# Performance work log

Measured on AMD Instinct MI355X. Metric: run time of the kernel, lower is better.

The kernel has to match this reference:

```python
import jax, jax.numpy as jnp
import numpy as np

# Model config (matches init_kwargs)
DIM = 2048
INTER = 1408          # moe_inter_dim
E = 16                # n_routed_experts
TOPK = 4              # n_activated_experts
G = 4                 # n_expert_groups
TOPK_G = 2            # n_limited_groups
N_SHARED = 2
SHARED_INTER = N_SHARED * INTER  # 2816
ROUTE_SCALE = 1.0


def setup_inputs() -> dict:
    key = jax.random.key(0)
    ks = jax.random.split(key, 8)
    s = 0.02
    x = jax.random.normal(ks[0], (1, 2048, DIM), dtype=jnp.float32)
    Wg = jax.random.normal(ks[1], (E, DIM), dtype=jnp.float32) * s      # gate weight
    W1 = jax.random.normal(ks[2], (E, INTER, DIM), dtype=jnp.float32) * s  # expert gate proj
    W3 = jax.random.normal(ks[3], (E, INTER, DIM), dtype=jnp.float32) * s  # expert up proj
    W2 = jax.random.normal(ks[4], (E, DIM, INTER), dtype=jnp.float32) * s  # expert down proj
    Ws1 = jax.random.normal(ks[5], (SHARED_INTER, DIM), dtype=jnp.float32) * s
    Ws3 = jax.random.normal(ks[6], (SHARED_INTER, DIM), dtype=jnp.float32) * s
    Ws2 = jax.random.normal(ks[7], (DIM, SHARED_INTER), dtype=jnp.float32) * s
    return {"x": x, "Wg": Wg, "W1": W1, "W3": W3, "W2": W2,
            "Ws1": Ws1, "Ws3": Ws3, "Ws2": Ws2}


def _moe_forward(x, Wg, W1, W3, W2, Ws1, Ws3, Ws2):
    B, S, D = x.shape
    xt = x.reshape(-1, D)              # [T, D]
    T = xt.shape[0]

    # ---- Gate: group-limited top-k routing (bias is None since dim != 7168) ----
    scores = jax.nn.softmax(xt @ Wg.T, axis=-1)          # [T, E]
    sg = scores.reshape(T, G, E // G)                    # [T, G, E/G]
    group_scores = sg.max(axis=-1)                       # amax per group
    gidx = jax.lax.top_k(group_scores, TOPK_G)[1]        # [T, TOPK_G]
    gmask = jax.nn.one_hot(gidx, G, dtype=jnp.float32).sum(axis=1) > 0  # [T, G] kept groups
    masked = jnp.where(gmask[:, :, None], sg, -jnp.inf).reshape(T, E)
    topi = jax.lax.top_k(masked, TOPK)[1]                # [T, TOPK] expert indices
    weights = jnp.take_along_axis(scores, topi, axis=1) * ROUTE_SCALE  # original_scores gather

    # ---- Routed experts: dense per-expert SwiGLU FFN, zero-weight combine ----
    # combine[t, e] = sum over k of weights[t, k] * (topi[t, k] == e)
    combine = jnp.zeros((T, E), xt.dtype).at[jnp.arange(T)[:, None], topi].add(weights)
    h = jax.nn.silu(jnp.einsum('td,eid->eti', xt, W1)) * jnp.einsum('td,eid->eti', xt, W3)
    expert_out = jnp.einsum('eti,edi->etd', h, W2)       # [E, T, D]
    y = jnp.einsum('etd,te->td', expert_out, combine)    # [T, D]

    # ---- Shared expert (applied to all tokens) ----
    z = (jax.nn.silu(xt @ Ws1.T) * (xt @ Ws3.T)) @ Ws2.T

    return (y + z).reshape(B, S, D)


def reference(x, Wg, W1, W3, W2, Ws1, Ws3, Ws2):
    return _moe_forward(x, Wg, W1, W3, W2, Ws1, Ws3, Ws2)
```

## Files before the change

### kernel.cpp

```cpp
#include <hip/hip_runtime.h>
#include <stdint.h>

#define D_MODEL  2048
#define N_INTER  1408
#define SH_INTER 2816
#define T_TOK    2048
#define NSLOT    (T_TOK * 4)
#define MIB(x)   ((size_t)(x) << 20)

typedef __attribute__((ext_vector_type(8))) short bf16x8;
typedef __attribute__((ext_vector_type(4))) float f32x4;

__device__ __forceinline__ unsigned short f2bf(float f){
  unsigned int b = __builtin_bit_cast(unsigned int, f);
  b = (b + 0x7FFFu + ((b >> 16) & 1u)) >> 16;
  return (unsigned short)b;
}
__device__ __forceinline__ float bf2f(unsigned short h){
  unsigned int b = ((unsigned int)h) << 16;
  return __builtin_bit_cast(float, b);
}

#define GLOAD16(gp, lp) __builtin_amdgcn_global_load_lds( \
    (const __attribute__((address_space(1))) unsigned int*)(gp), \
    (__attribute__((address_space(3))) unsigned int*)(lp), 16, 0, 0)

__global__ void cvt_bf16_kernel(const float* __restrict__ x,
                                unsigned short* __restrict__ o, int n4){
  const int stride = gridDim.x * blockDim.x;
  for (int i = blockIdx.x * blockDim.x + threadIdx.x; i < n4; i += stride){
    const float4 v = ((const float4*)x)[i];
    ushort4 u; u.x = f2bf(v.x); u.y = f2bf(v.y); u.z = f2bf(v.z); u.w = f2bf(v.w);
    ((ushort4*)o)[i] = u;
  }
}

__global__ void gate_kernel(const float* __restrict__ x, const float* __restrict__ Wg,
                            int* __restrict__ cnt, int* __restrict__ list,
                            float* __restrict__ wslot){
  const int t = blockIdx.x;
  const int l = threadIdx.x;
  const int e = l & 15, q = l >> 4;
  const float* xr = x + (size_t)t * D_MODEL + q * 512;
  const float* wr = Wg + (size_t)e * D_MODEL + q * 512;
  float p = 0.f;
  #pragma unroll 4
  for (int i = 0; i < 512; i += 4){
    float4 xv = *(const float4*)(xr + i);
    float4 wv = *(const float4*)(wr + i);
    p += xv.x*wv.x + xv.y*wv.y + xv.z*wv.z + xv.w*wv.w;
  }
  p += __shfl_xor(p, 16);
  p += __shfl_xor(p, 32);
  float mx = p;
  for (int d = 1; d < 16; d <<= 1) mx = fmaxf(mx, __shfl_xor(mx, d));
  float ex = __expf(p - mx);
  float sum = ex;
  for (int d = 1; d < 16; d <<= 1) sum += __shfl_xor(sum, d);
  const float sc = ex / sum;
  float gm = fmaxf(sc, __shfl_xor(sc, 1));
  gm = fmaxf(gm, __shfl_xor(gm, 2));
  const float g0 = __shfl(gm, 0), g1 = __shfl(gm, 4),
              g2 = __shfl(gm, 8), g3 = __shfl(gm, 12);
  const int grp = e >> 2;
  const float gs[4] = {g0, g1, g2, g3};
  int grank = 0;
  #pragma unroll
  for (int j = 0; j < 4; ++j)
    if (gs[j] > gm || (gs[j] == gm && j < grp)) grank++;
  const float msc = (grank < 2) ? sc : -INFINITY;
  int erank = 0;
  #pragma unroll
  for (int j = 0; j < 16; ++j){
    const float oj = __shfl(msc, j);
    if (oj > msc || (oj == msc && j < e)) erank++;
  }
  if (q == 0 && erank < 4 && msc > -INFINITY){
    const int pos = atomicAdd(&cnt[e], 1);
    const int slot = (t << 2) | erank;
    list[e * T_TOK + pos] = slot;
    wslot[slot] = sc;
  }
}

template<int MODE>
__global__ __launch_bounds__(256, 3)
void gemm6_kernel(const unsigned short* __restrict__ A,
                  const unsigned short* __restrict__ B,
                  void* __restrict__ OutP,
                  const int* __restrict__ list,
                  const int* __restrict__ cnt,
                  int N, int K, int Astride, int MT, int NT)
{
  constexpr bool GATHER = (MODE >= 2);
  __shared__ unsigned short As[3 * 128 * 32];
  __shared__ unsigned short Bs[3 * 128 * 32];

  const int per = gridDim.x >> 3;
  const int gsw = (blockIdx.x & 7) * per + (blockIdx.x >> 3);
  const int mt   = gsw % MT;
  const int rest = gsw / MT;
  const int nt = GATHER ? (rest % NT) : rest;
  const int e  = GATHER ? (rest / NT) : 0;

  const int cntE = GATHER ? cnt[e] : (MT * 128);
  if (mt * 128 >= cntE) return;

  const int tid = threadIdx.x, wid = tid >> 6, lane = tid & 63;

  const int rt0 = 32 * wid + (lane >> 2), rt1 = rt0 + 16;
  const int sxA = ((lane & 3) ^ ((lane >> 3) & 3)) << 3;

  int ar0, ar1;
  if constexpr (GATHER){
    const int lim = cntE - 1;
    int p0 = mt * 128 + rt0; p0 = p0 < lim ? p0 : lim;
    int p1 = mt * 128 + rt1; p1 = p1 < lim ? p1 : lim;
    const int e0 = list[e * T_TOK + p0], e1 = list[e * T_TOK + p1];
    ar0 = (MODE == 2) ? (e0 >> 2) : e0;
    ar1 = (MODE == 2) ? (e1 >> 2) : e1;
  } else { ar0 = mt * 128 + rt0; ar1 = mt * 128 + rt1; }

  const unsigned short* pa0 = A + (size_t)ar0 * Astride + sxA;
  const unsigned short* pa1 = A + (size_t)ar1 * Astride + sxA;
  const unsigned short* pb0 = B + (GATHER ? (size_t)e * N * K : 0)
                            + (size_t)(nt * 128 + rt0) * K + sxA;
  const unsigned short* pb1 = pb0 + (size_t)16 * K;

  const int aW0 = (32 * wid) * 32, aW1 = aW0 + 16 * 32;
  const int bufStride = 128 * 32;

  const int wr = wid >> 1, wc = wid & 1, lr = lane & 15, lq = lane >> 4;
  const int fx = ((lq ^ ((lr >> 1) & 3)) << 3);
  int aoff[4], boff[4];
  #pragma unroll
  for (int m = 0; m < 4; ++m) aoff[m] = (wr * 64 + m * 16 + lr) * 32 + fx;
  #pragma unroll
  for (int n = 0; n < 4; ++n) boff[n] = (wc * 64 + n * 16 + lr) * 32 + fx;

  f32x4 acc[4][4];
  const f32x4 zero = {0.f, 0.f, 0.f, 0.f};
  #pragma unroll
  for (int m = 0; m < 4; ++m)
    #pragma unroll
    for (int n = 0; n < 4; ++n) acc[m][n] = zero;

  const int KT = K >> 5;
  #pragma unroll
  for (int t = 0; t < 3; ++t){
    GLOAD16(pa0, As + t * bufStride + aW0);
    GLOAD16(pa1, As + t * bufStride + aW1);
    GLOAD16(pb0, Bs + t * bufStride + aW0);
    GLOAD16(pb1, Bs + t * bufStride + aW1);
    pa0 += 32; pa1 += 32; pb0 += 32; pb1 += 32;
  }
  int c = 0;

  for (int kt = 0; kt < KT; ++kt){
    if (kt < KT - 2)       asm volatile("s_waitcnt vmcnt(8)" ::: "memory");
    else if (kt == KT - 2) asm volatile("s_waitcnt vmcnt(4)" ::: "memory");
    else                   asm volatile("s_waitcnt vmcnt(0)" ::: "memory");
    __builtin_amdgcn_s_barrier();

    const unsigned short* aC = As + c * bufStride;
    const unsigned short* bC = Bs + c * bufStride;
    bf16x8 af[4], bf[4];
    #pragma unroll
    for (int m = 0; m < 4; ++m) af[m] = *(const bf16x8*)(aC + aoff[m]);
    #pragma unroll
    for (int n = 0; n < 4; ++n) bf[n] = *(const bf16x8*)(bC + boff[n]);

    asm volatile("s_waitcnt lgkmcnt(0)" ::: "memory");
    __builtin_amdgcn_sched_barrier(0);
    __builtin_amdgcn_s_barrier();

    if (kt + 3 < KT){
      GLOAD16(pa0, As + c * bufStride + aW0);
      GLOAD16(pa1, As + c * bufStride + aW1);
      GLOAD16(pb0, Bs + c * bufStride + aW0);
      GLOAD16(pb1, Bs + c * bufStride + aW1);
      pa0 += 32; pa1 += 32; pb0 += 32; pb1 += 32;
    }

    #pragma unroll
    for (int n = 0; n < 4; ++n)
      #pragma unroll
      for (int m = 0; m < 4; ++m)
        acc[m][n] = __builtin_amdgcn_mfma_f32_16x16x32_bf16(af[m], bf[n], acc[m][n], 0, 0, 0);

    c = (c == 2) ? 0 : c + 1;
  }

  const int colBase = nt * 128 + wc * 64;
  #pragma unroll
  for (int m = 0; m < 4; ++m){
    #pragma unroll
    for (int r = 0; r < 4; ++r){
      const int grow = mt * 128 + wr * 64 + m * 16 + lq * 4 + r;
      if constexpr (MODE == 1){
        float* op = (float*)OutP + (size_t)grow * N + colBase;
        #pragma unroll
        for (int n = 0; n < 4; ++n) op[n * 16 + lr] = acc[m][n][r];
      } else if constexpr (MODE == 0){
        unsigned short* op = (unsigned short*)OutP + (size_t)grow * N + colBase;
        #pragma unroll
        for (int n = 0; n < 4; ++n) op[n * 16 + lr] = f2bf(acc[m][n][r]);
      } else {
        if (grow >= cntE) continue;
        const int orow = list[e * T_TOK + grow];
        unsigned short* op = (unsigned short*)OutP + (size_t)orow * N + colBase;
        #pragma unroll
        for (int n = 0; n < 4; ++n) op[n * 16 + lr] = f2bf(acc[m][n][r]);
      }
    }
  }
}

__global__ void swiglu_ip_kernel(unsigned short* __restrict__ GU, int n8, int NI8){
  const int stride = gridDim.x * blockDim.x;
  bf16x8* p = (bf16x8*)GU;
  for (int i = blockIdx.x * blockDim.x + threadIdx.x; i < n8; i += stride){
    const int r = i / NI8, ccol = i - r * NI8;
    const size_t gi = (size_t)r * 2 * NI8 + ccol;
    const bf16x8 g = p[gi];
    const bf16x8 u = p[gi + NI8];
    bf16x8 h;
    #pragma unroll
    for (int j = 0; j < 8; ++j){
      const float gv = bf2f((unsigned short)g[j]);
      const float uv = bf2f((unsigned short)u[j]);
      h[j] = (short)f2bf(gv / (1.f + __expf(-gv)) * uv);
    }
    p[gi] = h;
  }
}

__global__ void swiglu2_kernel(unsigned short* __restrict__ G,
                               const unsigned short* __restrict__ U, int n8){
  const int stride = gridDim.x * blockDim.x;
  for (int i = blockIdx.x * blockDim.x + threadIdx.x; i < n8; i += stride){
    const bf16x8 g = ((const bf16x8*)G)[i];
    const bf16x8 u = ((const bf16x8*)U)[i];
    bf16x8 h;
    #pragma unroll
    for (int j = 0; j < 8; ++j){
      const float gv = bf2f((unsigned short)g[j]);
      const float uv = bf2f((unsigned short)u[j]);
      h[j] = (short)f2bf(gv / (1.f + __expf(-gv)) * uv);
    }
    ((bf16x8*)G)[i] = h;
  }
}

__global__ void combine_kernel(const unsigned short* __restrict__ H2,
                               const float* __restrict__ wslot,
                               float* __restrict__ out){
  const int t = blockIdx.x;
  const int ccol = threadIdx.x * 8;
  float w[4];
  #pragma unroll
  for (int k = 0; k < 4; ++k) w[k] = wslot[t * 4 + k];
  float* o = out + (size_t)t * D_MODEL + ccol;
  float a[8];
  #pragma unroll
  for (int j = 0; j < 8; ++j) a[j] = o[j];
  #pragma unroll
  for (int k = 0; k < 4; ++k){
    const bf16x8 hv = *(const bf16x8*)(H2 + (size_t)(t * 4 + k) * D_MODEL + ccol);
    #pragma unroll
    for (int j = 0; j < 8; ++j) a[j] += w[k] * bf2f((unsigned short)hv[j]);
  }
  #pragma unroll
  for (int j = 0; j < 8; ++j) o[j] = a[j];
}

extern "C" void kernel_launch(void* const* d_in, const int* in_sizes, int n_in,
                              void* d_out, int out_size, void* d_ws, size_t ws_size,
                              hipStream_t stream)
{
  const float* x   = (const float*)d_in[0];
  const float* Wg  = (const float*)d_in[1];
  const float* W1  = (const float*)d_in[2];
  const float* W3  = (const float*)d_in[3];
  const float* W2  = (const float*)d_in[4];
  const float* Ws1 = (const float*)d_in[5];
  const float* Ws3 = (const float*)d_in[6];
  const float* Ws2 = (const float*)d_in[7];
  float* out = (float*)d_out;

  char* ws = (char*)d_ws;
  int*   cnt   = (int*)(ws);
  int*   list  = (int*)(ws + 4096);
  float* wslot = (float*)(ws + 4096 + 131072);
  unsigned short* xbf  = (unsigned short*)(ws + MIB(1));
  unsigned short* H2   = (unsigned short*)(ws + MIB(1));
  unsigned short* GU_s = (unsigned short*)(ws + MIB(9));
  unsigned short* Ubuf = (unsigned short*)(ws + MIB(9));
  unsigned short* Wb   = (unsigned short*)(ws + MIB(33));
  unsigned short* Gbuf = (unsigned short*)(ws + MIB(121));
  unsigned short* Wb2  = Wb + (size_t)SH_INTER * D_MODEL;

  hipMemsetAsync(cnt, 0, 4096, stream);
  cvt_bf16_kernel<<<2048, 256, 0, stream>>>(x, xbf, T_TOK * D_MODEL / 4);
  gate_kernel<<<T_TOK, 64, 0, stream>>>(x, Wg, cnt, list, wslot);

  cvt_bf16_kernel<<<4096, 256, 0, stream>>>(Ws1, Wb,  SH_INTER * D_MODEL / 4);
  cvt_bf16_kernel<<<4096, 256, 0, stream>>>(Ws3, Wb2, SH_INTER * D_MODEL / 4);
  gemm6_kernel<0><<<16 * 44, 256, 0, stream>>>(xbf, Wb, GU_s, nullptr, nullptr,
                                               2 * SH_INTER, D_MODEL, D_MODEL, 16, 44);
  swiglu_ip_kernel<<<2048, 256, 0, stream>>>(GU_s, T_TOK * SH_INTER / 8, SH_INTER / 8);
  cvt_bf16_kernel<<<4096, 256, 0, stream>>>(Ws2, Wb, D_MODEL * SH_INTER / 4);
  gemm6_kernel<1><<<16 * 16, 256, 0, stream>>>(GU_s, Wb, out, nullptr, nullptr,
                                               D_MODEL, SH_INTER, 2 * SH_INTER, 16, 16);

  cvt_bf16_kernel<<<8192, 256, 0, stream>>>(W1, Wb, 16 * N_INTER * D_MODEL / 4);
  gemm6_kernel<2><<<16 * 11 * 16, 256, 0, stream>>>(xbf, Wb, Gbuf, list, cnt,
                                                    N_INTER, D_MODEL, D_MODEL, 16, 11);
  cvt_bf16_kernel<<<8192, 256, 0, stream>>>(W3, Wb, 16 * N_INTER * D_MODEL / 4);
  gemm6_kernel<2><<<16 * 11 * 16, 256, 0, stream>>>(xbf, Wb, Ubuf, list, cnt,
                                                    N_INTER, D_MODEL, D_MODEL, 16, 11);
  swiglu2_kernel<<<2048, 256, 0, stream>>>(Gbuf, Ubuf, NSLOT * N_INTER / 8);
  cvt_bf16_kernel<<<8192, 256, 0, stream>>>(W2, Wb, 16 * D_MODEL * N_INTER / 4);
  gemm6_kernel<3><<<16 * 16 * 16, 256, 0, stream>>>(Gbuf, Wb, H2, list, cnt,
                                                    D_MODEL, N_INTER, N_INTER, 16, 16);
  combine_kernel<<<T_TOK, 256, 0, stream>>>(H2, wslot, out);
}
```

Baseline: 604.5 us.

## Move to 256x256 GEMM tiles with fused gate/up, split-K shared down, merged conversions

Replaces the 128x128 GEMM with a 512-thread 256x256-tile variant that raises MFMA priority during the compute phase. The routed W1 and W3 projections are fused into one gathered GEMM whose output holds both halves. The shared down-projection uses 4-way split-K into fp32 partials, which the combine kernel now sums. The x and shared-weight conversions are merged into one launch, and each weight gets its own bf16 buffer instead of reusing one scratch area. These changes aim to cut launch count, improve operand reuse and fill the GPU better, at the cost of more workspace, extra partial-sum traffic, and register pressure from 32 accumulators per thread.

```diff
diff --git a/kernel.cpp b/kernel.cpp
--- a/kernel.cpp
+++ b/kernel.cpp
@@ -32,6 +32,26 @@
     const float4 v = ((const float4*)x)[i];
     ushort4 u; u.x = f2bf(v.x); u.y = f2bf(v.y); u.z = f2bf(v.z); u.w = f2bf(v.w);
     ((ushort4*)o)[i] = u;
+  }
+}
+
+__global__ void cvt4_kernel(const float* __restrict__ x,  const float* __restrict__ Ws1,
+                            const float* __restrict__ Ws3, const float* __restrict__ Ws2,
+                            unsigned short* __restrict__ xbf, unsigned short* __restrict__ S1,
+                            unsigned short* __restrict__ S3,  unsigned short* __restrict__ S2){
+  const int N0 = T_TOK * D_MODEL / 4;
+  const int NW = SH_INTER * D_MODEL / 4;
+  const int total = N0 + 3 * NW;
+  const int stride = gridDim.x * blockDim.x;
+  for (int i = blockIdx.x * blockDim.x + threadIdx.x; i < total; i += stride){
+    const float4* s; ushort4* d; int j;
+    if (i < N0)            { s = (const float4*)x;   d = (ushort4*)xbf; j = i; }
+    else if (i < N0 + NW)  { s = (const float4*)Ws1; d = (ushort4*)S1;  j = i - N0; }
+    else if (i < N0 + 2*NW){ s = (const float4*)Ws3; d = (ushort4*)S3;  j = i - N0 - NW; }
+    else                   { s = (const float4*)Ws2; d = (ushort4*)S2;  j = i - N0 - 2*NW; }
+    const float4 v = s[j];
+    ushort4 u; u.x = f2bf(v.x); u.y = f2bf(v.y); u.z = f2bf(v.z); u.w = f2bf(v.w);
+    d[j] = u;
   }
 }
 
@@ -83,75 +103,87 @@
   }
 }
 
-template<int MODE>
-__global__ __launch_bounds__(256, 3)
-void gemm6_kernel(const unsigned short* __restrict__ A,
-                  const unsigned short* __restrict__ B,
+template<int MODE, int KS>
+__global__ __launch_bounds__(512, 2)
+void gemm8_kernel(const unsigned short* __restrict__ A,
+                  const unsigned short* __restrict__ BG,
+                  const unsigned short* __restrict__ BU,
                   void* __restrict__ OutP,
                   const int* __restrict__ list,
                   const int* __restrict__ cnt,
-                  int N, int K, int Astride, int MT, int NT)
+                  int K, int N, int NI, int MT, int NT)
 {
-  constexpr bool GATHER = (MODE >= 2);
-  __shared__ unsigned short As[3 * 128 * 32];
-  __shared__ unsigned short Bs[3 * 128 * 32];
+  constexpr bool GATHER = (MODE == 2 || MODE == 3);
+  constexpr bool GU     = (MODE == 0 || MODE == 2);
+  __shared__ unsigned short As[3 * 8192];
+  __shared__ unsigned short Bs[3 * 8192];
 
   const int per = gridDim.x >> 3;
   const int gsw = (blockIdx.x & 7) * per + (blockIdx.x >> 3);
-  const int mt   = gsw % MT;
+  const int mt = gsw % MT;
   const int rest = gsw / MT;
-  const int nt = GATHER ? (rest % NT) : rest;
-  const int e  = GATHER ? (rest / NT) : 0;
-
-  const int cntE = GATHER ? cnt[e] : (MT * 128);
-  if (mt * 128 >= cntE) return;
+  const int nt = rest % NT;
+  const int rest2 = rest / NT;
+  const int ks = (KS > 1) ? (rest2 % KS) : 0;
+  const int e  = GATHER ? rest2 : 0;
+  const int cntE = GATHER ? cnt[e] : (MT * 256);
+  if (mt * 256 >= cntE) return;
 
   const int tid = threadIdx.x, wid = tid >> 6, lane = tid & 63;
+  const int sx   = ((lane & 3) ^ ((lane >> 3) & 3)) << 3;
+  const int kOff = (KS > 1) ? ks * (K / KS) : 0;
 
   const int rt0 = 32 * wid + (lane >> 2), rt1 = rt0 + 16;
-  const int sxA = ((lane & 3) ^ ((lane >> 3) & 3)) << 3;
-
   int ar0, ar1;
-  if constexpr (GATHER){
+  if (GATHER){
     const int lim = cntE - 1;
-    int p0 = mt * 128 + rt0; p0 = p0 < lim ? p0 : lim;
-    int p1 = mt * 128 + rt1; p1 = p1 < lim ? p1 : lim;
+    int p0 = mt * 256 + rt0; p0 = p0 < lim ? p0 : lim;
+    int p1 = mt * 256 + rt1; p1 = p1 < lim ? p1 : lim;
     const int e0 = list[e * T_TOK + p0], e1 = list[e * T_TOK + p1];
     ar0 = (MODE == 2) ? (e0 >> 2) : e0;
     ar1 = (MODE == 2) ? (e1 >> 2) : e1;
-  } else { ar0 = mt * 128 + rt0; ar1 = mt * 128 + rt1; }
-
-  const unsigned short* pa0 = A + (size_t)ar0 * Astride + sxA;
-  const unsigned short* pa1 = A + (size_t)ar1 * Astride + sxA;
-  const unsigned short* pb0 = B + (GATHER ? (size_t)e * N * K : 0)
-                            + (size_t)(nt * 128 + rt0) * K + sxA;
-  const unsigned short* pb1 = pb0 + (size_t)16 * K;
-
-  const int aW0 = (32 * wid) * 32, aW1 = aW0 + 16 * 32;
-  const int bufStride = 128 * 32;
-
-  const int wr = wid >> 1, wc = wid & 1, lr = lane & 15, lq = lane >> 4;
-  const int fx = ((lq ^ ((lr >> 1) & 3)) << 3);
-  int aoff[4], boff[4];
-  #pragma unroll
-  for (int m = 0; m < 4; ++m) aoff[m] = (wr * 64 + m * 16 + lr) * 32 + fx;
-  #pragma unroll
-  for (int n = 0; n < 4; ++n) boff[n] = (wc * 64 + n * 16 + lr) * 32 + fx;
-
-  f32x4 acc[4][4];
+  } else { ar0 = mt * 256 + rt0; ar1 = mt * 256 + rt1; }
+  const unsigned short* pa0 = A + (size_t)ar0 * K + kOff + sx;
+  const unsigned short* pa1 = A + (size_t)ar1 * K + kOff + sx;
+
+  const unsigned short* pb0;
+  const unsigned short* pb1;
+  if (GU){
+    const size_t eo = GATHER ? (size_t)e * NI * K : 0;
+    const int g0 = nt * 256 + rt0, g1 = nt * 256 + rt1;
+    pb0 = (g0 < NI ? BG + eo + (size_t)g0 * K : BU + eo + (size_t)(g0 - NI) * K) + sx;
+    pb1 = (g1 < NI ? BG + eo + (size_t)g1 * K : BU + eo + (size_t)(g1 - NI) * K) + sx;
+  } else {
+    const unsigned short* base = BG + (GATHER ? (size_t)e * N * K : 0) + kOff;
+    pb0 = base + (size_t)(nt * 256 + rt0) * K + sx;
+    pb1 = base + (size_t)(nt * 256 + rt1) * K + sx;
+  }
+
+  const int w0 = (32 * wid) * 32, w1 = w0 + 512;
+  const int bufStr = 8192;
+
+  const int wm = wid >> 2, wn = wid & 3, lr = lane & 15, lq = lane >> 4;
+  const int fx = (lq ^ ((lr >> 1) & 3)) << 3;
+  int aoff[8], boff[4];
+  #pragma unroll
+  for (int m = 0; m < 8; ++m) aoff[m] = (wm * 128 + m * 16 + lr) * 32 + fx;
+  #pragma unroll
+  for (int n = 0; n < 4; ++n) boff[n] = (wn * 64 + n * 16 + lr) * 32 + fx;
+
+  f32x4 acc[8][4];
   const f32x4 zero = {0.f, 0.f, 0.f, 0.f};
   #pragma unroll
-  for (int m = 0; m < 4; ++m)
+  for (int m = 0; m < 8; ++m)
     #pragma unroll
     for (int n = 0; n < 4; ++n) acc[m][n] = zero;
 
-  const int KT = K >> 5;
+  const int KT = (K / (KS > 1 ? KS : 1)) >> 5;
   #pragma unroll
   for (int t = 0; t < 3; ++t){
-    GLOAD16(pa0, As + t * bufStride + aW0);
-    GLOAD16(pa1, As + t * bufStride + aW1);
-    GLOAD16(pb0, Bs + t * bufStride + aW0);
-    GLOAD16(pb1, Bs + t * bufStride + aW1);
+    GLOAD16(pa0, As + t * bufStr + w0);
+    GLOAD16(pa1, As + t * bufStr + w1);
+    GLOAD16(pb0, Bs + t * bufStr + w0);
+    GLOAD16(pb1, Bs + t * bufStr + w1);
     pa0 += 32; pa1 += 32; pb0 += 32; pb1 += 32;
   }
   int c = 0;
@@ -162,11 +194,11 @@
     else                   asm volatile("s_waitcnt vmcnt(0)" ::: "memory");
     __builtin_amdgcn_s_barrier();
 
-    const unsigned short* aC = As + c * bufStride;
-    const unsigned short* bC = Bs + c * bufStride;
-    bf16x8 af[4], bf[4];
-    #pragma unroll
-    for (int m = 0; m < 4; ++m) af[m] = *(const bf16x8*)(aC + aoff[m]);
+    const unsigned short* aC = As + c * bufStr;
+    const unsigned short* bC = Bs + c * bufStr;
+    bf16x8 af[8], bf[4];
+    #pragma unroll
+    for (int m = 0; m < 8; ++m) af[m] = *(const bf16x8*)(aC + aoff[m]);
     #pragma unroll
     for (int n = 0; n < 4; ++n) bf[n] = *(const bf16x8*)(bC + boff[n]);
 
@@ -175,33 +207,35 @@
     __builtin_amdgcn_s_barrier();
 
     if (kt + 3 < KT){
-      GLOAD16(pa0, As + c * bufStride + aW0);
-      GLOAD16(pa1, As + c * bufStride + aW1);
-      GLOAD16(pb0, Bs + c * bufStride + aW0);
-      GLOAD16(pb1, Bs + c * bufStride + aW1);
+      GLOAD16(pa0, As + c * bufStr + w0);
+      GLOAD16(pa1, As + c * bufStr + w1);
+      GLOAD16(pb0, Bs + c * bufStr + w0);
+      GLOAD16(pb1, Bs + c * bufStr + w1);
       pa0 += 32; pa1 += 32; pb0 += 32; pb1 += 32;
     }
 
+    __builtin_amdgcn_s_setprio(1);
     #pragma unroll
     for (int n = 0; n < 4; ++n)
       #pragma unroll
-      for (int m = 0; m < 4; ++m)
+      for (int m = 0; m < 8; ++m)
         acc[m][n] = __builtin_amdgcn_mfma_f32_16x16x32_bf16(af[m], bf[n], acc[m][n], 0, 0, 0);
+    __builtin_amdgcn_s_setprio(0);
 
     c = (c == 2) ? 0 : c + 1;
   }
 
-  const int colBase = nt * 128 + wc * 64;
-  #pragma unroll
-  for (int m = 0; m < 4; ++m){
+  const int colBase = nt * 256 + wn * 64;
+  #pragma unroll
+  for (int m = 0; m < 8; ++m){
     #pragma unroll
     for (int r = 0; r < 4; ++r){
-      const int grow = mt * 128 + wr * 64 + m * 16 + lq * 4 + r;
-      if constexpr (MODE == 1){
-        float* op = (float*)OutP + (size_t)grow * N + colBase;
+      const int grow = mt * 256 + wm * 128 + m * 16 + lq * 4 + r;
+      if (MODE == 1){
+        float* op = (float*)OutP + (size_t)ks * MT * 256 * N + (size_t)grow * N + colBase;
         #pragma unroll
         for (int n = 0; n < 4; ++n) op[n * 16 + lr] = acc[m][n][r];
-      } else if constexpr (MODE == 0){
+      } else if (MODE == 0){
         unsigned short* op = (unsigned short*)OutP + (size_t)grow * N + colBase;
         #pragma unroll
         for (int n = 0; n < 4; ++n) op[n * 16 + lr] = f2bf(acc[m][n][r]);
@@ -216,14 +250,14 @@
   }
 }
 
-__global__ void swiglu_ip_kernel(unsigned short* __restrict__ GU, int n8, int NI8){
+__global__ void swiglu_split_kernel(const unsigned short* __restrict__ GU,
+                                    unsigned short* __restrict__ H,
+                                    int n8, int NI8){
   const int stride = gridDim.x * blockDim.x;
-  bf16x8* p = (bf16x8*)GU;
   for (int i = blockIdx.x * blockDim.x + threadIdx.x; i < n8; i += stride){
     const int r = i / NI8, ccol = i - r * NI8;
-    const size_t gi = (size_t)r * 2 * NI8 + ccol;
-    const bf16x8 g = p[gi];
-    const bf16x8 u = p[gi + NI8];
+    const bf16x8 g = ((const bf16x8*)GU)[(size_t)r * 2 * NI8 + ccol];
+    const bf16x8 u = ((const bf16x8*)GU)[(size_t)r * 2 * NI8 + NI8 + ccol];
     bf16x8 h;
     #pragma unroll
     for (int j = 0; j < 8; ++j){
@@ -231,28 +265,12 @@
       const float uv = bf2f((unsigned short)u[j]);
       h[j] = (short)f2bf(gv / (1.f + __expf(-gv)) * uv);
     }
-    p[gi] = h;
-  }
-}
-
-__global__ void swiglu2_kernel(unsigned short* __restrict__ G,
-                               const unsigned short* __restrict__ U, int n8){
-  const int stride = gridDim.x * blockDim.x;
-  for (int i = blockIdx.x * blockDim.x + threadIdx.x; i < n8; i += stride){
-    const bf16x8 g = ((const bf16x8*)G)[i];
-    const bf16x8 u = ((const bf16x8*)U)[i];
-    bf16x8 h;
-    #pragma unroll
-    for (int j = 0; j < 8; ++j){
-      const float gv = bf2f((unsigned short)g[j]);
-      const float uv = bf2f((unsigned short)u[j]);
-      h[j] = (short)f2bf(gv / (1.f + __expf(-gv)) * uv);
-    }
-    ((bf16x8*)G)[i] = h;
+    ((bf16x8*)H)[i] = h;
   }
 }
 
 __global__ void combine_kernel(const unsigned short* __restrict__ H2,
+                               const float* __restrict__ P,
                                const float* __restrict__ wslot,
                                float* __restrict__ out){
   const int t = blockIdx.x;
@@ -260,16 +278,22 @@
   float w[4];
   #pragma unroll
   for (int k = 0; k < 4; ++k) w[k] = wslot[t * 4 + k];
-  float* o = out + (size_t)t * D_MODEL + ccol;
   float a[8];
   #pragma unroll
-  for (int j = 0; j < 8; ++j) a[j] = o[j];
+  for (int j = 0; j < 8; ++j) a[j] = 0.f;
+  #pragma unroll
+  for (int p = 0; p < 4; ++p){
+    const float* pp = P + (size_t)(p * T_TOK + t) * D_MODEL + ccol;
+    #pragma unroll
+    for (int j = 0; j < 8; ++j) a[j] += pp[j];
+  }
   #pragma unroll
   for (int k = 0; k < 4; ++k){
     const bf16x8 hv = *(const bf16x8*)(H2 + (size_t)(t * 4 + k) * D_MODEL + ccol);
     #pragma unroll
     for (int j = 0; j < 8; ++j) a[j] += w[k] * bf2f((unsigned short)hv[j]);
   }
+  float* o = out + (size_t)t * D_MODEL + ccol;
   #pragma unroll
   for (int j = 0; j < 8; ++j) o[j] = a[j];
 }
@@ -293,35 +317,41 @@
   int*   list  = (int*)(ws + 4096);
   float* wslot = (float*)(ws + 4096 + 131072);
   unsigned short* xbf  = (unsigned short*)(ws + MIB(1));
-  unsigned short* H2   = (unsigned short*)(ws + MIB(1));
-  unsigned short* GU_s = (unsigned short*)(ws + MIB(9));
-  unsigned short* Ubuf = (unsigned short*)(ws + MIB(9));
-  unsigned short* Wb   = (unsigned short*)(ws + MIB(33));
-  unsigned short* Gbuf = (unsigned short*)(ws + MIB(121));
-  unsigned short* Wb2  = Wb + (size_t)SH_INTER * D_MODEL;
+  unsigned short* S1   = (unsigned short*)(ws + MIB(10));
+  unsigned short* S3   = (unsigned short*)(ws + MIB(22));
+  unsigned short* S2   = (unsigned short*)(ws + MIB(34));
+  unsigned short* Hs   = (unsigned short*)(ws + MIB(46));
+  unsigned short* GU_s = (unsigned short*)(ws + MIB(58));
+  unsigned short* Hr   = (unsigned short*)(ws + MIB(82));
+  unsigned short* Hc   = (unsigned short*)(ws + MIB(129));
+  unsigned short* H2   = (unsigned short*)(ws + MIB(153));
+  float*          P    = (float*)        (ws + MIB(187));
+  unsigned short* W1b  = (unsigned short*)(ws + MIB(255));
+  unsigned short* W3b  = (unsigned short*)(ws + MIB(348));
+  unsigned short* W2b  = (unsigned short*)(ws + MIB(441));
+
+  const int NW_R = 16 * N_INTER * D_MODEL / 4;
 
   hipMemsetAsync(cnt, 0, 4096, stream);
-  cvt_bf16_kernel<<<2048, 256, 0, stream>>>(x, xbf, T_TOK * D_MODEL / 4);
+  cvt4_kernel<<<2048, 256, 0, stream>>>(x, Ws1, Ws3, Ws2, xbf, S1, S3, S2);
   gate_kernel<<<T_TOK, 64, 0, stream>>>(x, Wg, cnt, list, wslot);
 
-  cvt_bf16_kernel<<<4096, 256, 0, stream>>>(Ws1, Wb,  SH_INTER * D_MODEL / 4);
-  cvt_bf16_kernel<<<4096, 256, 0, stream>>>(Ws3, Wb2, SH_INTER * D_MODEL / 4);
-  gemm6_kernel<0><<<16 * 44, 256, 0, stream>>>(xbf, Wb, GU_s, nullptr, nullptr,
-                                               2 * SH_INTER, D_MODEL, D_MODEL, 16, 44);
-  swiglu_ip_kernel<<<2048, 256, 0, stream>>>(GU_s, T_TOK * SH_INTER / 8, SH_INTER / 8);
-  cvt_bf16_kernel<<<4096, 256, 0, stream>>>(Ws2, Wb, D_MODEL * SH_INTER / 4);
-  gemm6_kernel<1><<<16 * 16, 256, 0, stream>>>(GU_s, Wb, out, nullptr, nullptr,
-                                               D_MODEL, SH_INTER, 2 * SH_INTER, 16, 16);
-
-  cvt_bf16_kernel<<<8192, 256, 0, stream>>>(W1, Wb, 16 * N_INTER * D_MODEL / 4);
-  gemm6_kernel<2><<<16 * 11 * 16, 256, 0, stream>>>(xbf, Wb, Gbuf, list, cnt,
-                                                    N_INTER, D_MODEL, D_MODEL, 16, 11);
-  cvt_bf16_kernel<<<8192, 256, 0, stream>>>(W3, Wb, 16 * N_INTER * D_MODEL / 4);
-  gemm6_kernel<2><<<16 * 11 * 16, 256, 0, stream>>>(xbf, Wb, Ubuf, list, cnt,
-                                                    N_INTER, D_MODEL, D_MODEL, 16, 11);
-  swiglu2_kernel<<<2048, 256, 0, stream>>>(Gbuf, Ubuf, NSLOT * N_INTER / 8);
-  cvt_bf16_kernel<<<8192, 256, 0, stream>>>(W2, Wb, 16 * D_MODEL * N_INTER / 4);
-  gemm6_kernel<3><<<16 * 16 * 16, 256, 0, stream>>>(Gbuf, Wb, H2, list, cnt,
-                                                    D_MODEL, N_INTER, N_INTER, 16, 16);
-  combine_kernel<<<T_TOK, 256, 0, stream>>>(H2, wslot, out);
-}
+  gemm8_kernel<0, 1><<<176, 512, 0, stream>>>(xbf, S1, S3, GU_s, nullptr, nullptr,
+                                              D_MODEL, 2 * SH_INTER, SH_INTER, 8, 22);
+  cvt_bf16_kernel<<<4096, 256, 0, stream>>>(W1, W1b, NW_R);
+  cvt_bf16_kernel<<<4096, 256, 0, stream>>>(W3, W3b, NW_R);
+  swiglu_split_kernel<<<2048, 256, 0, stream>>>(GU_s, Hs, T_TOK * SH_INTER / 8, SH_INTER / 8);
+
+  gemm8_kernel<1, 4><<<256, 512, 0, stream>>>(Hs, S2, nullptr, P, nullptr, nullptr,
+                                              SH_INTER, D_MODEL, 0, 8, 8);
+
+  gemm8_kernel<2, 1><<<1408, 512, 0, stream>>>(xbf, W1b, W3b, Hr, list, cnt,
+                                               D_MODEL, 2 * N_INTER, N_INTER, 8, 11);
+  cvt_bf16_kernel<<<4096, 256, 0, stream>>>(W2, W2b, NW_R);
+  swiglu_split_kernel<<<2048, 256, 0, stream>>>(Hr, Hc, NSLOT * N_INTER / 8, N_INTER / 8);
+
+  gemm8_kernel<3, 1><<<1024, 512, 0, stream>>>(Hc, W2b, nullptr, H2, list, cnt,
+                                               N_INTER, D_MODEL, 0, 8, 8);
+
+  combine_kernel<<<T_TOK, 256, 0, stream>>>(H2, P, wslot, out);
+}
```

Result: slower. 734.6 us (+21.5%).

## Double-buffer GEMM LDS, fuse input/shared weight conversions, give weights separate buffers

Applied to the files above, without the earlier changes.

The GEMM pipeline drops from three LDS stages to two, which shrinks shared memory so the launch bound can request 4 blocks per SM instead of 3. The bf16 conversion of x and the three shared-expert weight tensors is merged into one grid-stride kernel, and the routed weight conversions use fewer blocks. Each converted weight now gets its own workspace region instead of reusing a single buffer. The aim is higher occupancy and fewer launches, at the cost of less prefetch depth for hiding global-load latency and a much larger workspace footprint.

```diff
diff --git a/kernel.cpp b/kernel.cpp
--- a/kernel.cpp
+++ b/kernel.cpp
@@ -32,6 +32,26 @@
     const float4 v = ((const float4*)x)[i];
     ushort4 u; u.x = f2bf(v.x); u.y = f2bf(v.y); u.z = f2bf(v.z); u.w = f2bf(v.w);
     ((ushort4*)o)[i] = u;
+  }
+}
+
+__global__ void cvt4_kernel(const float* __restrict__ x,  const float* __restrict__ Ws1,
+                            const float* __restrict__ Ws3, const float* __restrict__ Ws2,
+                            unsigned short* __restrict__ xbf, unsigned short* __restrict__ S1,
+                            unsigned short* __restrict__ S3,  unsigned short* __restrict__ S2){
+  const int N0 = T_TOK * D_MODEL / 4;
+  const int NW = SH_INTER * D_MODEL / 4;
+  const int total = N0 + 3 * NW;
+  const int stride = gridDim.x * blockDim.x;
+  for (int i = blockIdx.x * blockDim.x + threadIdx.x; i < total; i += stride){
+    const float4* s; ushort4* d; int j;
+    if (i < N0)            { s = (const float4*)x;   d = (ushort4*)xbf; j = i; }
+    else if (i < N0 + NW)  { s = (const float4*)Ws1; d = (ushort4*)S1;  j = i - N0; }
+    else if (i < N0 + 2*NW){ s = (const float4*)Ws3; d = (ushort4*)S3;  j = i - N0 - NW; }
+    else                   { s = (const float4*)Ws2; d = (ushort4*)S2;  j = i - N0 - 2*NW; }
+    const float4 v = s[j];
+    ushort4 u; u.x = f2bf(v.x); u.y = f2bf(v.y); u.z = f2bf(v.z); u.w = f2bf(v.w);
+    d[j] = u;
   }
 }
 
@@ -84,7 +104,7 @@
 }
 
 template<int MODE>
-__global__ __launch_bounds__(256, 3)
+__global__ __launch_bounds__(256, 4)
 void gemm6_kernel(const unsigned short* __restrict__ A,
                   const unsigned short* __restrict__ B,
                   void* __restrict__ OutP,
@@ -93,8 +113,8 @@
                   int N, int K, int Astride, int MT, int NT)
 {
   constexpr bool GATHER = (MODE >= 2);
-  __shared__ unsigned short As[3 * 128 * 32];
-  __shared__ unsigned short Bs[3 * 128 * 32];
+  __shared__ unsigned short As[2 * 128 * 32];
+  __shared__ unsigned short Bs[2 * 128 * 32];
 
   const int per = gridDim.x >> 3;
   const int gsw = (blockIdx.x & 7) * per + (blockIdx.x >> 3);
@@ -147,7 +167,7 @@
 
   const int KT = K >> 5;
   #pragma unroll
-  for (int t = 0; t < 3; ++t){
+  for (int t = 0; t < 2; ++t){
     GLOAD16(pa0, As + t * bufStride + aW0);
     GLOAD16(pa1, As + t * bufStride + aW1);
     GLOAD16(pb0, Bs + t * bufStride + aW0);
@@ -157,9 +177,8 @@
   int c = 0;
 
   for (int kt = 0; kt < KT; ++kt){
-    if (kt < KT - 2)       asm volatile("s_waitcnt vmcnt(8)" ::: "memory");
-    else if (kt == KT - 2) asm volatile("s_waitcnt vmcnt(4)" ::: "memory");
-    else                   asm volatile("s_waitcnt vmcnt(0)" ::: "memory");
+    if (kt < KT - 1) asm volatile("s_waitcnt vmcnt(4)" ::: "memory");
+    else             asm volatile("s_waitcnt vmcnt(0)" ::: "memory");
     __builtin_amdgcn_s_barrier();
 
     const unsigned short* aC = As + c * bufStride;
@@ -174,7 +193,7 @@
     __builtin_amdgcn_sched_barrier(0);
     __builtin_amdgcn_s_barrier();
 
-    if (kt + 3 < KT){
+    if (kt + 2 < KT){
       GLOAD16(pa0, As + c * bufStride + aW0);
       GLOAD16(pa1, As + c * bufStride + aW1);
       GLOAD16(pb0, Bs + c * bufStride + aW0);
@@ -188,7 +207,7 @@
       for (int m = 0; m < 4; ++m)
         acc[m][n] = __builtin_amdgcn_mfma_f32_16x16x32_bf16(af[m], bf[n], acc[m][n], 0, 0, 0);
 
-    c = (c == 2) ? 0 : c + 1;
+    c ^= 1;
   }
 
   const int colBase = nt * 128 + wc * 64;
@@ -293,35 +312,43 @@
   int*   list  = (int*)(ws + 4096);
   float* wslot = (float*)(ws + 4096 + 131072);
   unsigned short* xbf  = (unsigned short*)(ws + MIB(1));
-  unsigned short* H2   = (unsigned short*)(ws + MIB(1));
-  unsigned short* GU_s = (unsigned short*)(ws + MIB(9));
-  unsigned short* Ubuf = (unsigned short*)(ws + MIB(9));
-  unsigned short* Wb   = (unsigned short*)(ws + MIB(33));
-  unsigned short* Gbuf = (unsigned short*)(ws + MIB(121));
-  unsigned short* Wb2  = Wb + (size_t)SH_INTER * D_MODEL;
+  unsigned short* S1   = (unsigned short*)(ws + MIB(10));
+  unsigned short* S3   = S1 + (size_t)SH_INTER * D_MODEL;
+  unsigned short* S2   = (unsigned short*)(ws + MIB(34));
+  unsigned short* GU_s = (unsigned short*)(ws + MIB(46));
+  unsigned short* Gbuf = (unsigned short*)(ws + MIB(70));
+  unsigned short* Ubuf = (unsigned short*)(ws + MIB(94));
+  unsigned short* H2   = (unsigned short*)(ws + MIB(118));
+  unsigned short* W1b  = (unsigned short*)(ws + MIB(152));
+  unsigned short* W3b  = (unsigned short*)(ws + MIB(245));
+  unsigned short* W2b  = (unsigned short*)(ws + MIB(338));
+
+  const int NW_R = 16 * N_INTER * D_MODEL / 4;
 
   hipMemsetAsync(cnt, 0, 4096, stream);
-  cvt_bf16_kernel<<<2048, 256, 0, stream>>>(x, xbf, T_TOK * D_MODEL / 4);
+  cvt4_kernel<<<2048, 256, 0, stream>>>(x, Ws1, Ws3, Ws2, xbf, S1, S3, S2);
   gate_kernel<<<T_TOK, 64, 0, stream>>>(x, Wg, cnt, list, wslot);
 
-  cvt_bf16_kernel<<<4096, 256, 0, stream>>>(Ws1, Wb,  SH_INTER * D_MODEL / 4);
-  cvt_bf16_kernel<<<4096, 256, 0, stream>>>(Ws3, Wb2, SH_INTER * D_MODEL / 4);
-  gemm6_kernel<0><<<16 * 44, 256, 0, stream>>>(xbf, Wb, GU_s, nullptr, nullptr,
-                                               2 * SH_INTER, D_MODEL, D_MODEL, 16, 44);
+  gemm6_kernel<0><<<704, 256, 0, stream>>>(xbf, S1, GU_s, nullptr, nullptr,
+                                           2 * SH_INTER, D_MODEL, D_MODEL, 16, 44);
   swiglu_ip_kernel<<<2048, 256, 0, stream>>>(GU_s, T_TOK * SH_INTER / 8, SH_INTER / 8);
-  cvt_bf16_kernel<<<4096, 256, 0, stream>>>(Ws2, Wb, D_MODEL * SH_INTER / 4);
-  gemm6_kernel<1><<<16 * 16, 256, 0, stream>>>(GU_s, Wb, out, nullptr, nullptr,
-                                               D_MODEL, SH_INTER, 2 * SH_INTER, 16, 16);
-
-  cvt_bf16_kernel<<<8192, 256, 0, stream>>>(W1, Wb, 16 * N_INTER * D_MODEL / 4);
-  gemm6_kernel<2><<<16 * 11 * 16, 256, 0, stream>>>(xbf, Wb, Gbuf, list, cnt,
-                                                    N_INTER, D_MODEL, D_MODEL, 16, 11);
-  cvt_bf16_kernel<<<8192, 256, 0, stream>>>(W3, Wb, 16 * N_INTER * D_MODEL / 4);
-  gemm6_kernel<2><<<16 * 11 * 16, 256, 0, stream>>>(xbf, Wb, Ubuf, list, cnt,
-                                                    N_INTER, D_MODEL, D_MODEL, 16, 11);
+
+  gemm6_kernel<1><<<256, 256, 0, stream>>>(GU_s, S2, out, nullptr, nullptr,
+                                           D_MODEL, SH_INTER, 2 * SH_INTER, 16, 16);
+
+  cvt_bf16_kernel<<<4096, 256, 0, stream>>>(W1, W1b, NW_R);
+  cvt_bf16_kernel<<<4096, 256, 0, stream>>>(W3, W3b, NW_R);
+
+  gemm6_kernel<2><<<2816, 256, 0, stream>>>(xbf, W1b, Gbuf, list, cnt,
+                                            N_INTER, D_MODEL, D_MODEL, 16, 11);
+  gemm6_kernel<2><<<2816, 256, 0, stream>>>(xbf, W3b, Ubuf, list, cnt,
+                                            N_INTER, D_MODEL, D_MODEL, 16, 11);
   swiglu2_kernel<<<2048, 256, 0, stream>>>(Gbuf, Ubuf, NSLOT * N_INTER / 8);
-  cvt_bf16_kernel<<<8192, 256, 0, stream>>>(W2, Wb, 16 * D_MODEL * N_INTER / 4);
-  gemm6_kernel<3><<<16 * 16 * 16, 256, 0, stream>>>(Gbuf, Wb, H2, list, cnt,
-                                                    D_MODEL, N_INTER, N_INTER, 16, 16);
+
+  cvt_bf16_kernel<<<4096, 256, 0, stream>>>(W2, W2b, NW_R);
+
+  gemm6_kernel<3><<<4096, 256, 0, stream>>>(Gbuf, W2b, H2, list, cnt,
+                                            D_MODEL, N_INTER, N_INTER, 16, 16);
+
   combine_kernel<<<T_TOK, 256, 0, stream>>>(H2, wslot, out);
 }
```

After: 675.3 us. 1.12x slower.
